# Kernel optimization log

Measured on AMD Instinct MI355X. Metric: run time of the kernel, lower is better.

## Reference

```python
import jax, jax.numpy as jnp
import numpy as np

DIM = 512
HID = 1024        # dim * expansion_factor
QK = 128          # query_key_dim
G = 256           # group_size
EPS = 1e-5


def setup_inputs() -> dict:
    key = jax.random.key(0)
    ks = jax.random.split(key, 6)
    x = jax.random.normal(ks[0], (4, 4096, DIM), jnp.float32)
    ln_w = jnp.ones((DIM,), jnp.float32)
    ln_b = jnp.zeros((DIM,), jnp.float32)
    Wh = 0.02 * jax.random.normal(ks[1], (DIM, 2 * HID), jnp.float32)
    bh = jnp.zeros((2 * HID,), jnp.float32)
    Wqk = 0.02 * jax.random.normal(ks[2], (DIM, QK), jnp.float32)
    bqk = jnp.zeros((QK,), jnp.float32)
    gamma = 0.02 * jax.random.normal(ks[3], (4, QK), jnp.float32)  # nn.init.normal_(gamma, std=0.02)
    beta = jnp.zeros((4, QK), jnp.float32)
    Wo = 0.02 * jax.random.normal(ks[4], (HID, DIM), jnp.float32)
    bo = jnp.zeros((DIM,), jnp.float32)
    return {"x": x, "ln_w": ln_w, "ln_b": ln_b, "Wh": Wh, "bh": bh,
            "Wqk": Wqk, "bqk": bqk, "gamma": gamma, "beta": beta,
            "Wo": Wo, "bo": bo}


def reference(x, ln_w, ln_b, Wh, bh, Wqk, bqk, gamma, beta, Wo, bo):
    b, n, _ = x.shape
    g = n // G  # number of groups (n chosen as multiple of G -> no padding)

    # LayerNorm (torch uses biased variance)
    mu = jnp.mean(x, axis=-1, keepdims=True)
    var = jnp.mean((x - mu) ** 2, axis=-1, keepdims=True)
    normed = (x - mu) * jax.lax.rsqrt(var + EPS) * ln_w + ln_b

    # to_hidden: Linear -> SiLU, split into v / gate
    h = jax.nn.silu(normed @ Wh + bh)            # [b, n, 2*HID]
    v, gate = jnp.split(h, 2, axis=-1)           # each [b, n, HID]

    # to_qk: Linear -> SiLU, then 4-head offset/scale
    qk = jax.nn.silu(normed @ Wqk + bqk)         # [b, n, QK]
    qkh = qk[..., None, :] * gamma + beta        # [b, n, 4, QK]
    quad_q, lin_q, quad_k, lin_k = (qkh[..., i, :] for i in range(4))

    # group: b (g n) d -> b g n d
    grp = lambda t: t.reshape(b, g, G, t.shape[-1])
    qq, qk_, lq, lk, vv = map(grp, (quad_q, quad_k, lin_q, lin_k, v))

    # quadratic (group-local) attention with ReLU^2 scores, causal within group
    sim = jnp.einsum('bgid,bgjd->bgij', qq, qk_) / G
    attn = jnp.square(jnp.maximum(sim, 0.0))
    causal_mask = jnp.triu(jnp.ones((G, G), dtype=bool), 1)
    attn = jnp.where(causal_mask, 0.0, attn)
    quad_out = jnp.einsum('bgij,bgje->bgie', attn, vv)   # [b, g, G, HID]

    # linear attention across groups: per-group kv, exclusive cumsum over group dim
    lin_kv = jnp.einsum('bgnd,bgne->bgde', lk, vv) / G   # [b, g, QK, HID]
    lin_kv = jnp.cumsum(lin_kv, axis=1)
    lin_kv = jnp.pad(lin_kv, ((0, 0), (1, 0), (0, 0), (0, 0)))[:, :-1]
    lin_out = jnp.einsum('bgde,bgnd->bgne', lin_kv, lq)  # [b, g, G, HID]

    out = gate * (quad_out.reshape(b, n, HID) + lin_out.reshape(b, n, HID))
    return out @ Wo + bo + x
```

## Files before the change

kernel.cpp:

```cpp
#include <hip/hip_runtime.h>
#include <hip/hip_bf16.h>
#include <math.h>


#define BATCH 4
#define SEQ   4096
#define TROWS 16384
#define DIMD  512
#define HIDD  1024
#define QKD   128
#define GRP   256
#define NGRP  16
#define BGRP  64
#define EPIW  132
#define EPB   130

typedef unsigned short bfraw;
typedef __attribute__((ext_vector_type(8))) short bf16x8;
typedef __attribute__((ext_vector_type(8))) unsigned short u16x8;
typedef __attribute__((ext_vector_type(4))) unsigned int u32x4;
typedef __attribute__((ext_vector_type(4))) float f32x4;

__device__ __forceinline__ float bf2f(bfraw u) {
    union { float f; unsigned int i; } c;
    c.i = ((unsigned int)u) << 16;
    return c.f;
}
__device__ __forceinline__ bfraw f2bf(float f) {
    unsigned int x = __float_as_uint(f);
    unsigned int r = (x + 0x7fffu + ((x >> 16) & 1u)) >> 16;
    return (bfraw)r;
}
__device__ __forceinline__ unsigned int pkbf(float lo, float hi) {
    __hip_bfloat162 h2 = __float22bfloat162_rn(make_float2(lo, hi));
    union { __hip_bfloat162 h; unsigned int u; } c; c.h = h2;
    return c.u;
}
__device__ __forceinline__ void store16bf(bfraw* dst, const float* src) {
    u32x4 a, b;
    #pragma unroll
    for (int k = 0; k < 4; ++k) a[k] = pkbf(src[2 * k], src[2 * k + 1]);
    #pragma unroll
    for (int k = 0; k < 4; ++k) b[k] = pkbf(src[8 + 2 * k], src[8 + 2 * k + 1]);
    *(u32x4*)dst = a;
    *(u32x4*)(dst + 8) = b;
}
__device__ __forceinline__ float silu_f(float z) {
    return z / (1.f + __expf(-z));
}
__device__ __forceinline__ void gload_lds16(const void* g, void* l) {
    __builtin_amdgcn_global_load_lds(
        (const __attribute__((address_space(1))) unsigned int*)g,
        (__attribute__((address_space(3))) unsigned int*)l, 16, 0, 0);
}

__device__ __forceinline__ void mfma_step(const bfraw* As, const bfraw* Bs,
                                          f32x4 acc[4][4], int wm, int wn,
                                          int q, int mi) {
    bf16x8 af[4], bfg[4];
    #pragma unroll
    for (int i = 0; i < 4; ++i)
        af[i] = *(const bf16x8*)&As[(size_t)(wm * 64 + i * 16 + mi) * 32 + q * 8];
    #pragma unroll
    for (int j = 0; j < 4; ++j)
        bfg[j] = *(const bf16x8*)&Bs[(size_t)(wn * 64 + j * 16 + mi) * 32 + q * 8];
    #pragma unroll
    for (int i = 0; i < 4; ++i)
        #pragma unroll
        for (int j = 0; j < 4; ++j)
            acc[i][j] = __builtin_amdgcn_mfma_f32_16x16x32_bf16(af[i], bfg[j], acc[i][j], 0, 0, 0);
}

#define SMEMP_DECL                                              \
    __shared__ __align__(16) char smem_[33280];                 \
    bfraw* A0buf = (bfraw*)smem_;                               \
    bfraw* B0buf = (bfraw*)(smem_ + 8192);                      \
    bfraw* A1buf = (bfraw*)(smem_ + 16384);                     \
    bfraw* B1buf = (bfraw*)(smem_ + 24576);

#define PIPE_DSTS                                               \
    bfraw* a0d  = A0buf + wid * 512;                            \
    bfraw* a0d2 = A0buf + 2048 + wid * 512;                     \
    bfraw* b0d  = B0buf + wid * 512;                            \
    bfraw* b0d2 = B0buf + 2048 + wid * 512;                     \
    bfraw* a1d  = A1buf + wid * 512;                            \
    bfraw* a1d2 = A1buf + 2048 + wid * 512;                     \
    bfraw* b1d  = B1buf + wid * 512;                            \
    bfraw* b1d2 = B1buf + 2048 + wid * 512;

#define KLOOP_PRE(Abase, Astr, Bbase, Bstr)                                    \
    const bfraw* pa0 = (Abase) + (size_t)(t >> 2) * (Astr) + (t & 3) * 8;      \
    const bfraw* pa1 = pa0 + (size_t)64 * (Astr);                              \
    const bfraw* pb0 = (Bbase) + (size_t)(t >> 2) * (Bstr) + (t & 3) * 8;      \
    const bfraw* pb1 = pb0 + (size_t)64 * (Bstr);

#define STAGE0                                                                 \
    do { gload_lds16(pa0, a0d); gload_lds16(pa1, a0d2);                        \
         gload_lds16(pb0, b0d); gload_lds16(pb1, b0d2);                        \
         pa0 += 32; pa1 += 32; pb0 += 32; pb1 += 32; } while (0)
#define STAGE1                                                                 \
    do { gload_lds16(pa0, a1d); gload_lds16(pa1, a1d2);                        \
         gload_lds16(pb0, b1d); gload_lds16(pb1, b1d2);                        \
         pa0 += 32; pa1 += 32; pb0 += 32; pb1 += 32; } while (0)

#define PIPE_LOOP(NIT, Abase, Astr, Bbase, Bstr)                               \
    {                                                                          \
        KLOOP_PRE(Abase, Astr, Bbase, Bstr)                                    \
        STAGE0;                                                                \
        for (int it = 0; it < (NIT); it += 2) {                                \
            __syncthreads();                                                   \
            if (it + 1 < (NIT)) STAGE1;                                        \
            mfma_step(A0buf, B0buf, acc, wm, wn, q, mi);                       \
            __syncthreads();                                                   \
            if (it + 2 < (NIT)) STAGE0;                                        \
            if (it + 1 < (NIT))                                                \
                mfma_step(A1buf, B1buf, acc, wm, wn, q, mi);                   \
        }                                                                      \
        __syncthreads();                                                       \
    }

__device__ __forceinline__ int epi_row(int p, int lr) {
    return (lr < 16) ? (p * 16 + lr) : (64 + p * 16 + (lr - 16));
}

__global__ __launch_bounds__(256) void prep_kernel(const float* __restrict__ x,
                                                   const float* __restrict__ lnw,
                                                   const float* __restrict__ lnb,
                                                   const float* __restrict__ Wh,
                                                   const float* __restrict__ Wo,
                                                   const float* __restrict__ Wqk,
                                                   bfraw* __restrict__ normb,
                                                   bfraw* __restrict__ WhT,
                                                   bfraw* __restrict__ WoT,
                                                   bfraw* __restrict__ WqkT) {
    __shared__ float tile[32][33];
    int bid = blockIdx.x;
    int t = threadIdx.x;
    if (bid < 4096) {
        int row  = bid * 4 + (t >> 6);
        int lane = t & 63;
        const float* xr = x + (size_t)row * DIMD;
        float4 v0 = ((const float4*)xr)[lane];
        float4 v1 = ((const float4*)xr)[lane + 64];
        float s  = v0.x + v0.y + v0.z + v0.w + v1.x + v1.y + v1.z + v1.w;
        float ss = v0.x*v0.x + v0.y*v0.y + v0.z*v0.z + v0.w*v0.w
                 + v1.x*v1.x + v1.y*v1.y + v1.z*v1.z + v1.w*v1.w;
        #pragma unroll
        for (int off = 32; off; off >>= 1) {
            s  += __shfl_xor(s, off);
            ss += __shfl_xor(ss, off);
        }
        float mu  = s * (1.f / DIMD);
        float var = ss * (1.f / DIMD) - mu * mu;
        float inv = rsqrtf(var + 1e-5f);
        float4 w0 = ((const float4*)lnw)[lane],  w1 = ((const float4*)lnw)[lane + 64];
        float4 b0 = ((const float4*)lnb)[lane],  b1 = ((const float4*)lnb)[lane + 64];
        unsigned int o0 = pkbf((v0.x - mu) * inv * w0.x + b0.x,
                               (v0.y - mu) * inv * w0.y + b0.y);
        unsigned int o1 = pkbf((v0.z - mu) * inv * w0.z + b0.z,
                               (v0.w - mu) * inv * w0.w + b0.w);
        unsigned int o2 = pkbf((v1.x - mu) * inv * w1.x + b1.x,
                               (v1.y - mu) * inv * w1.y + b1.y);
        unsigned int o3 = pkbf((v1.z - mu) * inv * w1.z + b1.z,
                               (v1.w - mu) * inv * w1.w + b1.w);
        unsigned int* brow = (unsigned int*)(normb + (size_t)row * DIMD);
        ((uint2*)brow)[lane]      = make_uint2(o0, o1);
        ((uint2*)brow)[lane + 64] = make_uint2(o2, o3);
        return;
    }
    bid -= 4096;
    const float* in; bfraw* outp; int R, C, nx;
    if (bid < 1024)      { in = Wh;  outp = WhT;  R = DIMD; C = 2 * HIDD; nx = 64; }
    else if (bid < 1536) { bid -= 1024; in = Wo;  outp = WoT;  R = HIDD; C = DIMD; nx = 16; }
    else                 { bid -= 1536; in = Wqk; outp = WqkT; R = DIMD; C = QKD;  nx = 4; }
    int c0 = (bid % nx) * 32, r0 = (bid / nx) * 32;
    int tr = t >> 3, tc4 = (t & 7) * 4;
    float4 v = *(const float4*)&in[(size_t)(r0 + tr) * C + c0 + tc4];
    tile[tr][tc4 + 0] = v.x; tile[tr][tc4 + 1] = v.y;
    tile[tr][tc4 + 2] = v.z; tile[tr][tc4 + 3] = v.w;
    __syncthreads();
    ushort4 s;
    s.x = f2bf(tile[tc4 + 0][tr]);
    s.y = f2bf(tile[tc4 + 1][tr]);
    s.z = f2bf(tile[tc4 + 2][tr]);
    s.w = f2bf(tile[tc4 + 3][tr]);
    *(ushort4*)&outp[(size_t)(c0 + tr) * R + r0 + tc4] = s;
}

__global__ __launch_bounds__(256) void gemm_h(const bfraw* __restrict__ A,
                                              const bfraw* __restrict__ WhT,
                                              const bfraw* __restrict__ WqkT,
                                              const float* __restrict__ bias,
                                              const float* __restrict__ bqk,
                                              const float* __restrict__ gamma,
                                              const float* __restrict__ beta,
                                              bfraw* __restrict__ vT,
                                              bfraw* __restrict__ gate,
                                              bfraw* __restrict__ qq,
                                              bfraw* __restrict__ lq,
                                              bfraw* __restrict__ kk,
                                              bfraw* __restrict__ lkT) {
    SMEMP_DECL
    bfraw* epi2 = (bfraw*)smem_;
    float* epi = (float*)smem_;
    int t = threadIdx.x;
    int lane = t & 63, wid = t >> 6;
    int wm = wid >> 1, wn = wid & 1;
    int q = lane >> 4, mi = lane & 15;
    int row0 = blockIdx.y * 128, col0 = blockIdx.x * 128;
    bool is_qk = (blockIdx.x == 16);
    f32x4 acc[4][4] = {};
    PIPE_DSTS
    {
        const bfraw* Bbase = is_qk ? WqkT : (WhT + (size_t)col0 * DIMD);
        PIPE_LOOP(16, A + (size_t)row0 * DIMD, DIMD, Bbase, DIMD)
    }
    int bg = row0 >> 8;
    if (is_qk) {
        #pragma unroll
        for (int p = 0; p < 4; ++p) {
            #pragma unroll
            for (int j = 0; j < 4; ++j) {
                float bv = bqk[wn * 64 + j * 16 + mi];
                #pragma unroll
                for (int rg = 0; rg < 4; ++rg)
                    epi[(wm * 16 + q * 4 + rg) * EPIW + wn * 64 + j * 16 + mi] =
                        silu_f(acc[p][j][rg] + bv);
            }
            __syncthreads();
            {
                int lr = t >> 3, c0t = (t & 7) * 16;
                int gr = row0 + epi_row(p, lr);
                const float* src = &epi[lr * EPIW + c0t];
                float z[16];
                #pragma unroll
                for (int k = 0; k < 16; ++k) z[k] = src[k];
                #pragma unroll
                for (int hd = 0; hd < 3; ++hd) {
                    bfraw* arr = (hd == 0) ? qq : (hd == 1) ? lq : kk;
                    const float* gp = gamma + hd * QKD + c0t;
                    const float* ep = beta  + hd * QKD + c0t;
                    float tmp[16];
                    #pragma unroll
                    for (int k = 0; k < 16; ++k) tmp[k] = z[k] * gp[k] + ep[k];
                    store16bf(arr + (size_t)gr * QKD + c0t, tmp);
                }
            }
            {
                int c = t >> 1, half = t & 1;
                float g3 = gamma[3 * QKD + c], e3 = beta[3 * QKD + c];
                int j0 = (row0 & 255) + half * 64 + p * 16;
                float tmp[16];
                #pragma unroll
                for (int k = 0; k < 16; ++k)
                    tmp[k] = epi[(half * 16 + k) * EPIW + c] * g3 + e3;
                store16bf(lkT + ((size_t)bg * QKD + c) * GRP + j0, tmp);
            }
            __syncthreads();
        }
        return;
    }
    #pragma unroll
    for (int p = 0; p < 4; ++p)
        #pragma unroll
        for (int j = 0; j < 4; ++j) {
            float bv = bias[col0 + wn * 64 + j * 16 + mi];
            #pragma unroll
            for (int rg = 0; rg < 4; ++rg) {
                int rowl = wm * 64 + p * 16 + q * 4 + rg;
                epi2[rowl * EPB + wn * 64 + j * 16 + mi] = f2bf(silu_f(acc[p][j][rg] + bv));
            }
        }
    __syncthreads();
    if (col0 < HIDD) {
        int e2 = t & 63, jblk = t >> 6;
        const unsigned int* ep32 = (const unsigned int*)epi2;
        unsigned int wv[32];
        #pragma unroll
        for (int jj = 0; jj < 32; ++jj)
            wv[jj] = ep32[(size_t)(jblk * 32 + jj) * 65 + e2];
        int jbase = (row0 & 255) + jblk * 32;
        bfraw* dst0 = vT + ((size_t)bg * HIDD + col0 + 2 * e2) * GRP + jbase;
        bfraw* dst1 = dst0 + GRP;
        #pragma unroll
        for (int vq = 0; vq < 4; ++vq) {
            u16x8 s;
            #pragma unroll
            for (int k = 0; k < 8; ++k) s[k] = (bfraw)(wv[vq * 8 + k] & 0xffffu);
            *(u16x8*)(dst0 + vq * 8) = s;
        }
        #pragma unroll
        for (int vq = 0; vq < 4; ++vq) {
            u16x8 s;
            #pragma unroll
            for (int k = 0; k < 8; ++k) s[k] = (bfraw)(wv[vq * 8 + k] >> 16);
            *(u16x8*)(dst1 + vq * 8) = s;
        }
    } else {
        int lr = t >> 1, seg = t & 1;
        const bfraw* src = epi2 + (size_t)lr * EPB + seg * 64;
        bfraw* dst = gate + (size_t)(row0 + lr) * HIDD + (col0 - HIDD) + seg * 64;
        #pragma unroll
        for (int vq = 0; vq < 8; ++vq)
            *(u16x8*)(dst + vq * 8) = *(const u16x8*)(src + vq * 8);
    }
}

__global__ __launch_bounds__(256) void simkv_kernel(const bfraw* __restrict__ qq,
                                                    const bfraw* __restrict__ kk,
                                                    bfraw* __restrict__ attn,
                                                    const bfraw* __restrict__ vT,
                                                    const bfraw* __restrict__ lkT,
                                                    bfraw* __restrict__ kvT_raw) {
    SMEMP_DECL
    float* epi = (float*)smem_;
    int t = threadIdx.x;
    int lane = t & 63, wid = t >> 6;
    int wm = wid >> 1, wn = wid & 1;
    int q = lane >> 4, mi = lane & 15;
    int bid = blockIdx.x;
    f32x4 acc[4][4] = {};
    PIPE_DSTS
    if (bid < 512) {
        int bg = bid >> 3;
        int row0 = (bid & 7) * 128;
        PIPE_LOOP(8, vT + (size_t)bg * HIDD * GRP + (size_t)row0 * GRP, GRP,
                  lkT + (size_t)bg * QKD * GRP, GRP)
        bfraw* outg = kvT_raw + (size_t)bg * HIDD * QKD;
        #pragma unroll
        for (int p = 0; p < 4; ++p) {
            #pragma unroll
            for (int j = 0; j < 4; ++j)
                #pragma unroll
                for (int rg = 0; rg < 4; ++rg)
                    epi[(wm * 16 + q * 4 + rg) * EPIW + wn * 64 + j * 16 + mi] = acc[p][j][rg];
            __syncthreads();
            int lr = t >> 3, c0t = (t & 7) * 16;
            int gr = row0 + epi_row(p, lr);
            store16bf(outg + (size_t)gr * QKD + c0t, &epi[lr * EPIW + c0t]);
            __syncthreads();
        }
        return;
    }
    int i = bid - 512;
    int bg = i & 63;
    int tid = i >> 6;
    int ry = (tid == 0) ? 0 : 1;
    int rx = (tid == 2) ? 1 : 0;
    int row0 = ry * 128, col0 = rx * 128;
    PIPE_LOOP(4, qq + (size_t)(bg * GRP + row0) * QKD, QKD,
              kk + (size_t)(bg * GRP + col0) * QKD, QKD)
    bfraw* ag = attn + (size_t)bg * GRP * GRP;
    #pragma unroll
    for (int p = 0; p < 4; ++p) {
        #pragma unroll
        for (int j = 0; j < 4; ++j) {
            int colg = col0 + wn * 64 + j * 16 + mi;
            #pragma unroll
            for (int rg = 0; rg < 4; ++rg) {
                int rowg = row0 + wm * 64 + p * 16 + q * 4 + rg;
                float s = acc[p][j][rg] * (1.f / GRP);
                s = fmaxf(s, 0.f);
                s = s * s;
                epi[(wm * 16 + q * 4 + rg) * EPIW + wn * 64 + j * 16 + mi] =
                    (colg > rowg) ? 0.f : s;
            }
        }
        __syncthreads();
        int lr = t >> 3, c0t = (t & 7) * 16;
        int gr = row0 + epi_row(p, lr);
        store16bf(ag + (size_t)gr * GRP + col0 + c0t, &epi[lr * EPIW + c0t]);
        __syncthreads();
    }
}

__global__ __launch_bounds__(256) void cumsum2_kernel(const bfraw* __restrict__ raw,
                                                      bfraw* __restrict__ ex) {
    int idx = blockIdx.x * 256 + threadIdx.x;
    int b = idx >> 17;
    int r = idx & 131071;
    const bfraw* rp = raw + (size_t)b * NGRP * 131072 + r;
    bfraw* ep = ex + (size_t)b * NGRP * 131072 + r;
    float run = 0.f;
    #pragma unroll
    for (int g = 0; g < NGRP; ++g) {
        ep[(size_t)g * 131072] = f2bf(run);
        run += bf2f(rp[(size_t)g * 131072]) * (1.f / GRP);
    }
}

__global__ __launch_bounds__(256) void quadlin_mfma(const bfraw* __restrict__ attn,
                                                    const bfraw* __restrict__ vT,
                                                    const bfraw* __restrict__ lq,
                                                    const bfraw* __restrict__ kvT_ex,
                                                    const bfraw* __restrict__ gate,
                                                    bfraw* __restrict__ gated) {
    int bg = blockIdx.z;
    int row0 = blockIdx.y * 128;
    int col0 = blockIdx.x * 128;
    SMEMP_DECL
    float* epi = (float*)smem_;
    int t = threadIdx.x;
    int lane = t & 63, wid = t >> 6;
    int wm = wid >> 1, wn = wid & 1;
    int q = lane >> 4, mi = lane & 15;
    f32x4 acc[4][4] = {};
    PIPE_DSTS
    {
        int nit = (row0 + 128) >> 5;
        PIPE_LOOP(nit, attn + (size_t)bg * GRP * GRP + (size_t)row0 * GRP, GRP,
                  vT + (size_t)bg * HIDD * GRP + (size_t)col0 * GRP, GRP)
    }
    PIPE_LOOP(4, lq + (size_t)(bg * GRP + row0) * QKD, QKD,
              kvT_ex + (size_t)bg * HIDD * QKD + (size_t)col0 * QKD, QKD)
    #pragma unroll
    for (int p = 0; p < 4; ++p) {
        #pragma unroll
        for (int j = 0; j < 4; ++j)
            #pragma unroll
            for (int rg = 0; rg < 4; ++rg)
                epi[(wm * 16 + q * 4 + rg) * EPIW + wn * 64 + j * 16 + mi] = acc[p][j][rg];
        __syncthreads();
        int lr = t >> 3, c0t = (t & 7) * 16;
        int gr = row0 + epi_row(p, lr);
        size_t grow = (size_t)bg * GRP + gr;
        const float* src = &epi[lr * EPIW + c0t];
        const bfraw* gsrc = gate + grow * HIDD + col0 + c0t;
        u16x8 g0 = *(const u16x8*)gsrc;
        u16x8 g1 = *(const u16x8*)(gsrc + 8);
        float tmp[16];
        #pragma unroll
        for (int k = 0; k < 8; ++k) tmp[k] = src[k] * bf2f(g0[k]);
        #pragma unroll
        for (int k = 0; k < 8; ++k) tmp[8 + k] = src[8 + k] * bf2f(g1[k]);
        store16bf(gated + grow * HIDD + col0 + c0t, tmp);
        __syncthreads();
    }
}

__global__ __launch_bounds__(256) void gemm_final(const bfraw* __restrict__ A,
                                                  const bfraw* __restrict__ BT,
                                                  const float* __restrict__ bo,
                                                  const float* __restrict__ x,
                                                  float* __restrict__ out) {
    SMEMP_DECL
    float* epi = (float*)smem_;
    int t = threadIdx.x;
    int lane = t & 63, wid = t >> 6;
    int wm = wid >> 1, wn = wid & 1;
    int q = lane >> 4, mi = lane & 15;
    int row0 = blockIdx.y * 128, col0 = blockIdx.x * 128;
    f32x4 acc[4][4] = {};
    PIPE_DSTS
    PIPE_LOOP(32, A + (size_t)row0 * HIDD, HIDD, BT + (size_t)col0 * HIDD, HIDD)
    #pragma unroll
    for (int p = 0; p < 4; ++p) {
        #pragma unroll
        for (int j = 0; j < 4; ++j) {
            float bv = bo[col0 + wn * 64 + j * 16 + mi];
            #pragma unroll
            for (int rg = 0; rg < 4; ++rg)
                epi[(wm * 16 + q * 4 + rg) * EPIW + wn * 64 + j * 16 + mi] =
                    acc[p][j][rg] + bv;
        }
        __syncthreads();
        int lr = t >> 3, c0t = (t & 7) * 16;
        int gr = row0 + epi_row(p, lr);
        const float* src = &epi[lr * EPIW + c0t];
        const float* xsrc = x + (size_t)gr * DIMD + col0 + c0t;
        float* dst = out + (size_t)gr * DIMD + col0 + c0t;
        #pragma unroll
        for (int v = 0; v < 4; ++v) {
            float4 a = ((const float4*)src)[v];
            float4 xv = ((const float4*)xsrc)[v];
            a.x += xv.x; a.y += xv.y; a.z += xv.z; a.w += xv.w;
            ((float4*)dst)[v] = a;
        }
        __syncthreads();
    }
}

extern "C" void kernel_launch(void* const* d_in, const int* in_sizes, int n_in,
                              void* d_out, int out_size, void* d_ws, size_t ws_size,
                              hipStream_t stream) {
    const float* x     = (const float*)d_in[0];
    const float* ln_w  = (const float*)d_in[1];
    const float* ln_b  = (const float*)d_in[2];
    const float* Wh    = (const float*)d_in[3];
    const float* bh    = (const float*)d_in[4];
    const float* Wqk   = (const float*)d_in[5];
    const float* bqk   = (const float*)d_in[6];
    const float* gamma = (const float*)d_in[7];
    const float* beta  = (const float*)d_in[8];
    const float* Wo    = (const float*)d_in[9];
    const float* bo    = (const float*)d_in[10];
    float* out = (float*)d_out;

    char* outb_ = (char*)d_out;
    bfraw* attn = (bfraw*)(outb_);
    bfraw* qq   = (bfraw*)(outb_ + 8388608);
    bfraw* kk   = (bfraw*)(outb_ + 12582912);
    bfraw* lq   = (bfraw*)(outb_ + 16777216);
    bfraw* WhT  = (bfraw*)(outb_ + 20971520);
    bfraw* WqkT = (bfraw*)(outb_ + 23068672);

    char* wsb = (char*)d_ws;
    bfraw* vT      = (bfraw*)(wsb);
    bfraw* gate    = (bfraw*)(wsb + 33554432);
    bfraw* gated   = (bfraw*)(wsb + 67108864);
    bfraw* normb   = (bfraw*)(wsb + 100663296);
    bfraw* kvT_raw = (bfraw*)(wsb + 117440512);
    bfraw* kvT_ex  = (bfraw*)(wsb + 134217728);
    bfraw* lkT     = (bfraw*)(wsb + 150994944);
    bfraw* WoT     = (bfraw*)(wsb + 155189248);

    prep_kernel<<<4096 + 1024 + 512 + 64, 256, 0, stream>>>(
        x, ln_w, ln_b, Wh, Wo, Wqk, normb, WhT, WoT, WqkT);
    gemm_h<<<dim3(17, TROWS / 128), 256, 0, stream>>>(
        normb, WhT, WqkT, bh, bqk, gamma, beta, vT, gate, qq, lq, kk, lkT);
    simkv_kernel<<<512 + 192, 256, 0, stream>>>(qq, kk, attn, vT, lkT, kvT_raw);
    cumsum2_kernel<<<(BATCH * QKD * HIDD) / 256, 256, 0, stream>>>(kvT_raw, kvT_ex);
    quadlin_mfma<<<dim3(HIDD / 128, GRP / 128, BGRP), 256, 0, stream>>>(
        attn, vT, lq, kvT_ex, gate, gated);
    gemm_final<<<dim3(DIMD / 128, TROWS / 128), 256, 0, stream>>>(gated, WoT, bo, x, out);
}
```

Measured before the change: 279.3 us.

## Rewrite hidden projection GEMM with 256x256 tiles and 4-stage async LDS pipeline

Replaces the 128x128-tile hidden/qk projection GEMM with a 512-thread kernel that computes 256x256 tiles. It uses a 4-slot direct global-to-LDS load pipeline with swizzled LDS layout, explicit vmcnt waits and MFMA priority bumps. Block IDs are remapped across XCDs. The epilogue is restructured into four 64-row passes for the v-transpose, gate and qk outputs. Larger tiles raise operand reuse and cut redundant A loads, at the cost of 128KB of LDS per block. The qk tile also wastes compute: the 128-wide Wqk is padded to 256 columns.

```diff
diff --git a/kernel.cpp b/kernel.cpp
--- a/kernel.cpp
+++ b/kernel.cpp
@@ -187,122 +187,202 @@
     *(ushort4*)&outp[(size_t)(c0 + tr) * R + r0 + tc4] = s;
 }
 
-__global__ __launch_bounds__(256) void gemm_h(const bfraw* __restrict__ A,
-                                              const bfraw* __restrict__ WhT,
-                                              const bfraw* __restrict__ WqkT,
-                                              const float* __restrict__ bias,
-                                              const float* __restrict__ bqk,
-                                              const float* __restrict__ gamma,
-                                              const float* __restrict__ beta,
-                                              bfraw* __restrict__ vT,
-                                              bfraw* __restrict__ gate,
-                                              bfraw* __restrict__ qq,
-                                              bfraw* __restrict__ lq,
-                                              bfraw* __restrict__ kk,
-                                              bfraw* __restrict__ lkT) {
-    SMEMP_DECL
-    bfraw* epi2 = (bfraw*)smem_;
+__global__ __launch_bounds__(512, 2) void gemm_h256(
+    const bfraw* __restrict__ A,
+    const bfraw* __restrict__ WhT,
+    const bfraw* __restrict__ WqkT,
+    const float* __restrict__ bh,
+    const float* __restrict__ bqk,
+    const float* __restrict__ gamma,
+    const float* __restrict__ beta,
+    bfraw* __restrict__ vT,
+    bfraw* __restrict__ gate,
+    bfraw* __restrict__ qq,
+    bfraw* __restrict__ lq,
+    bfraw* __restrict__ kk,
+    bfraw* __restrict__ lkT) {
+    __shared__ __align__(16) char smem_[131072];
+    const int t = threadIdx.x;
+    const int lane = t & 63, wid = t >> 6;
+    const int wm = wid >> 2, wn = wid & 3;
+    const int q = lane >> 4, mi = lane & 15;
+    int nid = (blockIdx.x & 7) * 72 + (blockIdx.x >> 3);
+    const int ct = nid % 9, by = nid / 9;
+    const int r0 = by * 256, c0 = ct * 256;
+
+    const int lslot = (lane & 7) ^ (lane >> 3);
+    const int rbase = wid * 16 + (lane >> 3) * 2 + (lslot >> 2);
+    const int kel   = (lslot & 3) * 8;
+    const bfraw* As0 = A + (size_t)(r0 + rbase) * DIMD + kel;
+    const bfraw* As1 = As0 + (size_t)128 * DIMD;
+    const bfraw* Bs0; const bfraw* Bs1;
+    if (ct < 8) {
+        Bs0 = WhT + (size_t)(c0 + rbase) * DIMD + kel;
+        Bs1 = Bs0 + (size_t)128 * DIMD;
+    } else {
+        Bs0 = WqkT + (size_t)rbase * DIMD + kel;
+        Bs1 = Bs0;
+    }
+    const int swz = ((((mi & 1) << 2) | q) ^ ((mi >> 1) & 7)) << 4;
+    const int a_off = (wm * 64 + (mi >> 1)) * 128 + swz;
+    const int b_off = (wn * 32 + (mi >> 1)) * 128 + swz;
+    const int ldst = wid * 1024;
+
+#define GH_STAGE(KT, SLOT)                                                    \
+    do {                                                                      \
+        char* sb_ = smem_ + (SLOT) * 32768;                                   \
+        gload_lds16(As0 + (KT) * 32, sb_ + ldst);                             \
+        gload_lds16(As1 + (KT) * 32, sb_ + 8192 + ldst);                      \
+        gload_lds16(Bs0 + (KT) * 32, sb_ + 16384 + ldst);                     \
+        gload_lds16(Bs1 + (KT) * 32, sb_ + 24576 + ldst);                     \
+    } while (0)
+
+    f32x4 acc[8][4] = {};
+    GH_STAGE(0, 0);
+    GH_STAGE(1, 1);
+    GH_STAGE(2, 2);
+    asm volatile("s_waitcnt vmcnt(8)" ::: "memory");
+    __builtin_amdgcn_s_barrier();
+
+    #pragma unroll
+    for (int j = 0; j < 16; ++j) {
+        if (j + 3 < 16) GH_STAGE(j + 3, (j + 3) & 3);
+        const char* cb = smem_ + (j & 3) * 32768;
+        bf16x8 af[8], bfr[4];
+        #pragma unroll
+        for (int mf = 0; mf < 8; ++mf)
+            af[mf] = *(const bf16x8*)(cb + a_off + mf * 1024);
+        #pragma unroll
+        for (int nf = 0; nf < 4; ++nf)
+            bfr[nf] = *(const bf16x8*)(cb + 16384 + b_off + nf * 1024);
+        __builtin_amdgcn_s_setprio(1);
+        #pragma unroll
+        for (int mf = 0; mf < 8; ++mf)
+            #pragma unroll
+            for (int nf = 0; nf < 4; ++nf)
+                acc[mf][nf] = __builtin_amdgcn_mfma_f32_16x16x32_bf16(
+                    af[mf], bfr[nf], acc[mf][nf], 0, 0, 0);
+        __builtin_amdgcn_s_setprio(0);
+        if (j + 3 < 16)      asm volatile("s_waitcnt vmcnt(8)" ::: "memory");
+        else if (j + 2 < 16) asm volatile("s_waitcnt vmcnt(4)" ::: "memory");
+        else if (j + 1 < 16) asm volatile("s_waitcnt vmcnt(0)" ::: "memory");
+        __builtin_amdgcn_s_barrier();
+    }
+#undef GH_STAGE
+
     float* epi = (float*)smem_;
-    int t = threadIdx.x;
-    int lane = t & 63, wid = t >> 6;
-    int wm = wid >> 1, wn = wid & 1;
-    int q = lane >> 4, mi = lane & 15;
-    int row0 = blockIdx.y * 128, col0 = blockIdx.x * 128;
-    bool is_qk = (blockIdx.x == 16);
-    f32x4 acc[4][4] = {};
-    PIPE_DSTS
-    {
-        const bfraw* Bbase = is_qk ? WqkT : (WhT + (size_t)col0 * DIMD);
-        PIPE_LOOP(16, A + (size_t)row0 * DIMD, DIMD, Bbase, DIMD)
-    }
-    int bg = row0 >> 8;
-    if (is_qk) {
+    if (ct == 8) {
+        float* gbl = (float*)(smem_ + 33792);
+        gbl[t] = gamma[t];
+        gbl[t + 512] = beta[t];
+        float bq4[4];
+        #pragma unroll
+        for (int nf = 0; nf < 4; ++nf)
+            bq4[nf] = (wn < 2) ? bqk[wn * 64 + nf * 16 + mi] : 0.f;
         #pragma unroll
         for (int p = 0; p < 4; ++p) {
-            #pragma unroll
-            for (int j = 0; j < 4; ++j) {
-                float bv = bqk[wn * 64 + j * 16 + mi];
-                #pragma unroll
-                for (int rg = 0; rg < 4; ++rg)
-                    epi[(wm * 16 + q * 4 + rg) * EPIW + wn * 64 + j * 16 + mi] =
-                        silu_f(acc[p][j][rg] + bv);
+            if (wm == (p >> 1) && wn < 2) {
+                #pragma unroll
+                for (int m2 = 0; m2 < 4; ++m2) {
+                    int mf = ((p & 1) << 2) + m2;
+                    #pragma unroll
+                    for (int nf = 0; nf < 4; ++nf)
+                        #pragma unroll
+                        for (int rg = 0; rg < 4; ++rg)
+                            epi[(m2 * 16 + q * 4 + rg) * 132 + wn * 64 + nf * 16 + mi] =
+                                silu_f(acc[mf][nf][rg] + bq4[nf]);
+                }
             }
             __syncthreads();
             {
-                int lr = t >> 3, c0t = (t & 7) * 16;
-                int gr = row0 + epi_row(p, lr);
-                const float* src = &epi[lr * EPIW + c0t];
+                int lr = t >> 3, cs = (t & 7) * 16;
                 float z[16];
                 #pragma unroll
-                for (int k = 0; k < 16; ++k) z[k] = src[k];
+                for (int k = 0; k < 16; ++k) z[k] = epi[lr * 132 + cs + k];
+                size_t growr = (size_t)(r0 + p * 64 + lr) * QKD + cs;
                 #pragma unroll
                 for (int hd = 0; hd < 3; ++hd) {
                     bfraw* arr = (hd == 0) ? qq : (hd == 1) ? lq : kk;
-                    const float* gp = gamma + hd * QKD + c0t;
-                    const float* ep = beta  + hd * QKD + c0t;
                     float tmp[16];
                     #pragma unroll
-                    for (int k = 0; k < 16; ++k) tmp[k] = z[k] * gp[k] + ep[k];
-                    store16bf(arr + (size_t)gr * QKD + c0t, tmp);
+                    for (int k = 0; k < 16; ++k)
+                        tmp[k] = z[k] * gbl[hd * 128 + cs + k] + gbl[512 + hd * 128 + cs + k];
+                    store16bf(arr + growr, tmp);
                 }
             }
             {
-                int c = t >> 1, half = t & 1;
-                float g3 = gamma[3 * QKD + c], e3 = beta[3 * QKD + c];
-                int j0 = (row0 & 255) + half * 64 + p * 16;
+                int c = t >> 2, jh = (t & 3) * 16;
+                float g3 = gbl[384 + c], e3 = gbl[896 + c];
                 float tmp[16];
                 #pragma unroll
                 for (int k = 0; k < 16; ++k)
-                    tmp[k] = epi[(half * 16 + k) * EPIW + c] * g3 + e3;
-                store16bf(lkT + ((size_t)bg * QKD + c) * GRP + j0, tmp);
+                    tmp[k] = epi[(jh + k) * 132 + c] * g3 + e3;
+                store16bf(lkT + ((size_t)by * QKD + c) * GRP + p * 64 + jh, tmp);
             }
             __syncthreads();
         }
         return;
     }
-    #pragma unroll
-    for (int p = 0; p < 4; ++p)
-        #pragma unroll
-        for (int j = 0; j < 4; ++j) {
-            float bv = bias[col0 + wn * 64 + j * 16 + mi];
+    float bias4[4];
+    #pragma unroll
+    for (int nf = 0; nf < 4; ++nf)
+        bias4[nf] = bh[c0 + wn * 64 + nf * 16 + mi];
+    if (ct < 4) {
+        #pragma unroll
+        for (int p = 0; p < 4; ++p) {
+            if (wm == (p >> 1)) {
+                #pragma unroll
+                for (int m2 = 0; m2 < 4; ++m2) {
+                    int mf = ((p & 1) << 2) + m2;
+                    #pragma unroll
+                    for (int nf = 0; nf < 4; ++nf)
+                        #pragma unroll
+                        for (int rg = 0; rg < 4; ++rg)
+                            epi[(m2 * 16 + q * 4 + rg) * 257 + wn * 64 + nf * 16 + mi] =
+                                silu_f(acc[mf][nf][rg] + bias4[nf]);
+                }
+            }
+            __syncthreads();
+            int e2 = t >> 1, js = (t & 1) * 32;
+            bfraw* dst = vT + ((size_t)by * HIDD + c0 + e2) * GRP + p * 64 + js;
             #pragma unroll
-            for (int rg = 0; rg < 4; ++rg) {
-                int rowl = wm * 64 + p * 16 + q * 4 + rg;
-                epi2[rowl * EPB + wn * 64 + j * 16 + mi] = f2bf(silu_f(acc[p][j][rg] + bv));
-            }
-        }
-    __syncthreads();
-    if (col0 < HIDD) {
-        int e2 = t & 63, jblk = t >> 6;
-        const unsigned int* ep32 = (const unsigned int*)epi2;
-        unsigned int wv[32];
-        #pragma unroll
-        for (int jj = 0; jj < 32; ++jj)
-            wv[jj] = ep32[(size_t)(jblk * 32 + jj) * 65 + e2];
-        int jbase = (row0 & 255) + jblk * 32;
-        bfraw* dst0 = vT + ((size_t)bg * HIDD + col0 + 2 * e2) * GRP + jbase;
-        bfraw* dst1 = dst0 + GRP;
-        #pragma unroll
-        for (int vq = 0; vq < 4; ++vq) {
-            u16x8 s;
+            for (int h2 = 0; h2 < 2; ++h2) {
+                float tmp[16];
+                #pragma unroll
+                for (int k = 0; k < 16; ++k)
+                    tmp[k] = epi[(js + h2 * 16 + k) * 257 + e2];
+                store16bf(dst + h2 * 16, tmp);
+            }
+            __syncthreads();
+        }
+    } else {
+        #pragma unroll
+        for (int p = 0; p < 4; ++p) {
+            if (wm == (p >> 1)) {
+                #pragma unroll
+                for (int m2 = 0; m2 < 4; ++m2) {
+                    int mf = ((p & 1) << 2) + m2;
+                    #pragma unroll
+                    for (int nf = 0; nf < 4; ++nf)
+                        #pragma unroll
+                        for (int rg = 0; rg < 4; ++rg)
+                            epi[(m2 * 16 + q * 4 + rg) * 260 + wn * 64 + nf * 16 + mi] =
+                                silu_f(acc[mf][nf][rg] + bias4[nf]);
+                }
+            }
+            __syncthreads();
+            int lr = t >> 3, cs = (t & 7) * 32;
+            const float* src = epi + lr * 260 + cs;
+            bfraw* dst = gate + (size_t)(r0 + p * 64 + lr) * HIDD + (c0 - HIDD) + cs;
             #pragma unroll
-            for (int k = 0; k < 8; ++k) s[k] = (bfraw)(wv[vq * 8 + k] & 0xffffu);
-            *(u16x8*)(dst0 + vq * 8) = s;
-        }
-        #pragma unroll
-        for (int vq = 0; vq < 4; ++vq) {
-            u16x8 s;
-            #pragma unroll
-            for (int k = 0; k < 8; ++k) s[k] = (bfraw)(wv[vq * 8 + k] >> 16);
-            *(u16x8*)(dst1 + vq * 8) = s;
-        }
-    } else {
-        int lr = t >> 1, seg = t & 1;
-        const bfraw* src = epi2 + (size_t)lr * EPB + seg * 64;
-        bfraw* dst = gate + (size_t)(row0 + lr) * HIDD + (col0 - HIDD) + seg * 64;
-        #pragma unroll
-        for (int vq = 0; vq < 8; ++vq)
-            *(u16x8*)(dst + vq * 8) = *(const u16x8*)(src + vq * 8);
+            for (int h2 = 0; h2 < 2; ++h2) {
+                float tmp[16];
+                #pragma unroll
+                for (int k = 0; k < 16; ++k) tmp[k] = src[h2 * 16 + k];
+                store16bf(dst + h2 * 16, tmp);
+            }
+            __syncthreads();
+        }
     }
 }
 
@@ -516,7 +596,7 @@
 
     prep_kernel<<<4096 + 1024 + 512 + 64, 256, 0, stream>>>(
         x, ln_w, ln_b, Wh, Wo, Wqk, normb, WhT, WoT, WqkT);
-    gemm_h<<<dim3(17, TROWS / 128), 256, 0, stream>>>(
+    gemm_h256<<<576, 512, 0, stream>>>(
         normb, WhT, WqkT, bh, bqk, gamma, beta, vT, gate, qq, lq, kk, lkT);
     simkv_kernel<<<512 + 192, 256, 0, stream>>>(qq, kk, attn, vT, lkT, kvT_raw);
     cumsum2_kernel<<<(BATCH * QKD * HIDD) / 256, 256, 0, stream>>>(kvT_raw, kvT_ex);
```

Measured after the change: 278.5 us. About the same (-0.3%).
